# Kernel optimization log

Measured on AMD Instinct MI355X. Metric: run time of the kernel, lower is better.

Reference implementation:

```python
import jax, jax.numpy as jnp
import numpy as np

V = 25  # joints

def _normalize_adjacency_chain(adjacency: np.ndarray) -> np.ndarray:
    A = adjacency.astype(np.float32).copy()
    A += np.eye(A.shape[0], dtype=np.float32)
    row_sum = A.sum(axis=1, keepdims=True)
    row_sum[row_sum == 0.0] = 1.0
    return A / row_sum


def setup_inputs() -> dict:
    key = jax.random.key(0)
    k_x, k_w, k_b = jax.random.split(key, 3)
    N, C_in, C_out, T = 32, 256, 256, 300
    x = jax.random.normal(k_x, (N, C_in, V, T), dtype=jnp.float32)
    # chain adjacency over V joints, normalized with self-loops (module buffer)
    adj = np.zeros((V, V), dtype=np.float32)
    for i in range(V - 1):
        adj[i, i + 1] = 1.0
        adj[i + 1, i] = 1.0
    A = jnp.asarray(_normalize_adjacency_chain(adj))
    # 1x1 Conv2d params: weight (C_out, C_in), bias (C_out,)
    fan_in = C_in  # kernel 1x1
    bound = 1.0 / np.sqrt(fan_in)
    W = jax.random.uniform(k_w, (C_out, C_in), minval=-bound, maxval=bound, dtype=jnp.float32)
    b = jax.random.uniform(k_b, (C_out,), minval=-bound, maxval=bound, dtype=jnp.float32)
    return {"x": x, "A": A, "W": W, "b": b}


def reference(x, A, W, b):
    # x: (N, C, V, T); A: (V, V) row-normalized adjacency with self-loops
    agg = jnp.einsum('ncvt,vw->ncwt', x, A)          # graph aggregation
    out = jnp.einsum('ncvt,oc->novt', agg, W)        # 1x1 conv = channel GEMM
    return out + b[None, :, None, None]
```

## Files before the change

kernel.cpp:

```cpp
#include <hip/hip_runtime.h>

typedef unsigned short u16;
typedef unsigned int u32;
typedef __attribute__((ext_vector_type(8))) short short8;
typedef __attribute__((ext_vector_type(4))) float f32x4;
typedef __attribute__((ext_vector_type(2))) unsigned int u32x2;
typedef __attribute__((ext_vector_type(4))) unsigned int u32x4;

#define C_IN 256
#define C_OUT 256
#define VJ 25
#define TT 300
#define VT 7500
#define ROWBLKS 59
#define PERN_ELEMS (ROWBLKS * 4 * 128 * 64)
#define WB_ELEMS (256 * 256)

__device__ __forceinline__ u16 f2bf(float f) {
  u32 u = __float_as_uint(f);
  u32 r = (u + 0x7fffu + ((u >> 16) & 1u)) >> 16;
  return (u16)r;
}

__global__ void k0_wcast(const float* __restrict__ W, u16* __restrict__ Wb) {
  int i = (blockIdx.x * 256 + threadIdx.x) * 4;
  f32x4 w = *(const f32x4*)(W + i);
  u32x2 pk;
  pk[0] = (u32)f2bf(w[0]) | ((u32)f2bf(w[1]) << 16);
  pk[1] = (u32)f2bf(w[2]) | ((u32)f2bf(w[3]) << 16);
  *(u32x2*)(Wb + i) = pk;
}

__global__ __launch_bounds__(256) void k1_stencil(
    const float* __restrict__ x, const float* __restrict__ A,
    u16* __restrict__ aggT, int n0) {
  __shared__ float cw[25][4];
  __shared__ u16 agg_s[25 * 16 * 72];
  const int tid = threadIdx.x;
  const int tblk = blockIdx.x;
  const int cblk = blockIdx.y;
  const int nn = blockIdx.z;
  const int n = n0 + nn;

  if (tid < 25) {
    int w = tid;
    cw[w][0] = (w > 0) ? A[(w - 1) * 25 + w] : 0.0f;
    cw[w][1] = A[w * 25 + w];
    cw[w][2] = (w < 24) ? A[(w + 1) * 25 + w] : 0.0f;
  }
  __syncthreads();

  const int t_i = tid & 15;
  const int c_i = tid >> 4;
  const int t0 = tblk * 16 + t_i;
  const int tc = (t0 < TT) ? t0 : (TT - 1);

#pragma unroll
  for (int jp = 0; jp < 4; jp += 2) {
    const int cl = c_i * 4 + jp;
    const int c = cblk * 64 + cl;
    const float* xp0 = x + ((size_t)n * C_IN + c) * VT + tc;
    const float* xp1 = xp0 + VT;
    float xv0[25], xv1[25];
#pragma unroll
    for (int v = 0; v < 25; ++v) { xv0[v] = xp0[v * TT]; xv1[v] = xp1[v * TT]; }
#pragma unroll
    for (int w = 0; w < 25; ++w) {
      const int wm = (w > 0) ? w - 1 : 0;
      const int wp = (w < 24) ? w + 1 : 24;
      float a0 = cw[w][0], a1 = cw[w][1], a2 = cw[w][2];
      float r0 = xv0[wm] * a0 + xv0[w] * a1 + xv0[wp] * a2;
      float r1 = xv1[wm] * a0 + xv1[w] * a1 + xv1[wp] * a2;
      u32 pk = (u32)f2bf(r0) | ((u32)f2bf(r1) << 16);
      *(u32*)&agg_s[(w * 16 + t_i) * 72 + cl] = pk;
    }
  }
  __syncthreads();

  const int c8 = tid & 7;
  const int rb = tid >> 3;
  u16* dstn = aggT + (size_t)nn * PERN_ELEMS;
#pragma unroll
  for (int it = 0; it < 13; ++it) {
    int rr = it * 32 + rb;
    if (rr < 400) {
      int w = rr >> 4, ti = rr & 15;
      int t = tblk * 16 + ti;
      if (t < TT) {
        int g = w * TT + t;
        int rowblk = g >> 7, row_in = g & 127;
        u32x4 v = *(const u32x4*)&agg_s[(w * 16 + ti) * 72 + c8 * 8];
        *(u32x4*)(dstn + ((size_t)(rowblk * 4 + cblk) * 128 + row_in) * 64 + c8 * 8) = v;
      }
    }
  }
}

__global__ __launch_bounds__(256, 2) void k2_gemm(
    const u16* __restrict__ aggT, const u16* __restrict__ Wb,
    const float* __restrict__ bias, float* __restrict__ out, int n0) {
  __shared__ u16 As[128 * 64];
  __shared__ u16 Bs[128 * 64];
  const int tid = threadIdx.x;
  const int cb = blockIdx.x;
  const int ob = blockIdx.y;
  const int nn = blockIdx.z;
  const int n = n0 + nn;
  const int l = tid & 63;
  const int wv = tid >> 6;
  const int wm = wv & 1, wn = wv >> 1;
  const int m = l & 15, quad = l >> 4;
  f32x4 acc[4][4] = {};

  const u16* aggn = aggT + (size_t)nn * PERN_ELEMS + (size_t)cb * 4 * 8192;
  const u16* wbase = Wb + ob * 128 * 256;

  for (int kb = 0; kb < 4; ++kb) {
#pragma unroll
    for (int i = 0; i < 4; ++i) {
      int ch = i * 256 + tid;
      int row = ch >> 3, jp = ch & 7;
      int jd = jp ^ (row & 7);
      const u16* ga = wbase + row * 256 + kb * 64 + jd * 8;
      __builtin_amdgcn_global_load_lds((const __attribute__((address_space(1))) void*)ga,
                                       (__attribute__((address_space(3))) void*)&As[ch * 8],
                                       16, 0, 0);
      const u16* gb = aggn + kb * 8192 + row * 64 + jd * 8;
      __builtin_amdgcn_global_load_lds((const __attribute__((address_space(1))) void*)gb,
                                       (__attribute__((address_space(3))) void*)&Bs[ch * 8],
                                       16, 0, 0);
    }
    __syncthreads();
#pragma unroll
    for (int ks = 0; ks < 2; ++ks) {
      short8 af[4], bfr[4];
      int jj = ks * 4 + quad;
#pragma unroll
      for (int mi = 0; mi < 4; ++mi) {
        int row = wm * 64 + mi * 16 + m;
        af[mi] = *(const short8*)&As[row * 64 + ((jj ^ (row & 7)) * 8)];
      }
#pragma unroll
      for (int ni = 0; ni < 4; ++ni) {
        int row = wn * 64 + ni * 16 + m;
        bfr[ni] = *(const short8*)&Bs[row * 64 + ((jj ^ (row & 7)) * 8)];
      }
#pragma unroll
      for (int mi = 0; mi < 4; ++mi)
#pragma unroll
        for (int ni = 0; ni < 4; ++ni)
          acc[mi][ni] = __builtin_amdgcn_mfma_f32_16x16x32_bf16(af[mi], bfr[ni], acc[mi][ni], 0, 0, 0);
    }
    __syncthreads();
  }

  float* outn = out + (size_t)n * C_OUT * VT;
  const int colbase = cb * 128 + wn * 64 + m;
#pragma unroll
  for (int mi = 0; mi < 4; ++mi) {
    const int o0 = ob * 128 + wm * 64 + mi * 16 + quad * 4;
    float b0 = bias[o0], b1 = bias[o0 + 1], b2 = bias[o0 + 2], b3 = bias[o0 + 3];
#pragma unroll
    for (int ni = 0; ni < 4; ++ni) {
      int col = colbase + ni * 16;
      if (col < VT) {
        float* p = outn + (size_t)o0 * VT + col;
        p[0]          = acc[mi][ni][0] + b0;
        p[VT]         = acc[mi][ni][1] + b1;
        p[2 * VT]     = acc[mi][ni][2] + b2;
        p[3 * VT]     = acc[mi][ni][3] + b3;
      }
    }
  }
}

extern "C" void kernel_launch(void* const* d_in, const int* in_sizes, int n_in,
                              void* d_out, int out_size, void* d_ws, size_t ws_size,
                              hipStream_t stream) {
  (void)in_sizes; (void)n_in; (void)out_size;
  const float* x = (const float*)d_in[0];
  const float* A = (const float*)d_in[1];
  const float* W = (const float*)d_in[2];
  const float* b = (const float*)d_in[3];
  float* out = (float*)d_out;
  u16* wb = (u16*)d_ws;
  u16* aggT = wb + WB_ELEMS;

  const size_t pern_bytes = (size_t)PERN_ELEMS * 2;
  const size_t base_bytes = (size_t)WB_ELEMS * 2;
  int nchunk = 1;
  if (ws_size > base_bytes + pern_bytes) {
    size_t a = (ws_size - base_bytes) / pern_bytes;
    nchunk = (a >= 32) ? 32 : (int)a;
  }

  k0_wcast<<<64, 256, 0, stream>>>(W, wb);
  for (int n0 = 0; n0 < 32; n0 += nchunk) {
    int nc = 32 - n0; if (nc > nchunk) nc = nchunk;
    k1_stencil<<<dim3(19, 4, nc), 256, 0, stream>>>(x, A, aggT, n0);
    k2_gemm<<<dim3(59, 2, nc), 256, 0, stream>>>(aggT, wb, b, out, n0);
  }
}
```

Baseline: 514.5 us.

## Fuse graph stencil into GEMM, computing bf16 operands in registers

Replaces the separate stencil and GEMM kernels with one kernel where each lane computes the 3-tap graph aggregation directly from x and packs it into MFMA B fragments, while W fragments are loaded directly from global memory. This removes the workspace round trip of the bf16 intermediate and the per-chunk launches. It trades that for redundant neighbor loads of x, narrower x access segments, and no LDS staging of W, and it adds nontemporal output stores.

```diff
diff --git a/kernel.cpp b/kernel.cpp
--- a/kernel.cpp
+++ b/kernel.cpp
@@ -5,21 +5,15 @@
 typedef __attribute__((ext_vector_type(8))) short short8;
 typedef __attribute__((ext_vector_type(4))) float f32x4;
 typedef __attribute__((ext_vector_type(2))) unsigned int u32x2;
-typedef __attribute__((ext_vector_type(4))) unsigned int u32x4;
 
+#define TT 300
+#define VT 7500
 #define C_IN 256
 #define C_OUT 256
-#define VJ 25
-#define TT 300
-#define VT 7500
-#define ROWBLKS 59
-#define PERN_ELEMS (ROWBLKS * 4 * 128 * 64)
-#define WB_ELEMS (256 * 256)
 
 __device__ __forceinline__ u16 f2bf(float f) {
   u32 u = __float_as_uint(f);
-  u32 r = (u + 0x7fffu + ((u >> 16) & 1u)) >> 16;
-  return (u16)r;
+  return (u16)((u + 0x7fffu + ((u >> 16) & 1u)) >> 16);
 }
 
 __global__ void k0_wcast(const float* __restrict__ W, u16* __restrict__ Wb) {
@@ -31,144 +25,79 @@
   *(u32x2*)(Wb + i) = pk;
 }
 
-__global__ __launch_bounds__(256) void k1_stencil(
+__global__ __launch_bounds__(512) void k_fused(
     const float* __restrict__ x, const float* __restrict__ A,
-    u16* __restrict__ aggT, int n0) {
-  __shared__ float cw[25][4];
-  __shared__ u16 agg_s[25 * 16 * 72];
+    const u16* __restrict__ Wb, const float* __restrict__ bias,
+    float* __restrict__ out) {
   const int tid = threadIdx.x;
-  const int tblk = blockIdx.x;
-  const int cblk = blockIdx.y;
-  const int nn = blockIdx.z;
-  const int n = n0 + nn;
+  const int l = tid & 63, wv = tid >> 6;
+  const int gw = wv & 3, ow = wv >> 2;
+  const int quad = l >> 4, m16 = l & 15;
+  const int cb = blockIdx.x, n = blockIdx.y;
 
-  if (tid < 25) {
-    int w = tid;
-    cw[w][0] = (w > 0) ? A[(w - 1) * 25 + w] : 0.0f;
-    cw[w][1] = A[w * 25 + w];
-    cw[w][2] = (w < 24) ? A[(w + 1) * 25 + w] : 0.0f;
+  const float* xn = x + (size_t)n * C_IN * VT;
+
+  int gcol[2];
+  float ac[2][3];
+  const float* xb[2][3];
+#pragma unroll
+  for (int gt = 0; gt < 2; ++gt) {
+    int g = cb * 128 + gw * 32 + gt * 16 + m16;
+    gcol[gt] = g;
+    int gc = (g < VT) ? g : (VT - 1);
+    int w = gc / TT, t = gc - w * TT;
+    ac[gt][0] = (w > 0) ? A[(w - 1) * 25 + w] : 0.0f;
+    ac[gt][1] = A[w * 25 + w];
+    ac[gt][2] = (w < 24) ? A[(w + 1) * 25 + w] : 0.0f;
+    int wm = (w > 0) ? w - 1 : 0, wp = (w < 24) ? w + 1 : 24;
+    const float* base = xn + (size_t)(quad * 8) * VT + t;
+    xb[gt][0] = base + wm * TT;
+    xb[gt][1] = base + w * TT;
+    xb[gt][2] = base + wp * TT;
   }
-  __syncthreads();
 
-  const int t_i = tid & 15;
-  const int c_i = tid >> 4;
-  const int t0 = tblk * 16 + t_i;
-  const int tc = (t0 < TT) ? t0 : (TT - 1);
+  const u16* wrow = Wb + (size_t)(ow * 128 + m16) * C_IN + quad * 8;
 
+  f32x4 acc[8][2] = {};
+  for (int ks = 0; ks < 8; ++ks) {
+    short8 bf[2];
 #pragma unroll
-  for (int jp = 0; jp < 4; jp += 2) {
-    const int cl = c_i * 4 + jp;
-    const int c = cblk * 64 + cl;
-    const float* xp0 = x + ((size_t)n * C_IN + c) * VT + tc;
-    const float* xp1 = xp0 + VT;
-    float xv0[25], xv1[25];
+    for (int gt = 0; gt < 2; ++gt) {
 #pragma unroll
-    for (int v = 0; v < 25; ++v) { xv0[v] = xp0[v * TT]; xv1[v] = xp1[v * TT]; }
-#pragma unroll
-    for (int w = 0; w < 25; ++w) {
-      const int wm = (w > 0) ? w - 1 : 0;
-      const int wp = (w < 24) ? w + 1 : 24;
-      float a0 = cw[w][0], a1 = cw[w][1], a2 = cw[w][2];
-      float r0 = xv0[wm] * a0 + xv0[w] * a1 + xv0[wp] * a2;
-      float r1 = xv1[wm] * a0 + xv1[w] * a1 + xv1[wp] * a2;
-      u32 pk = (u32)f2bf(r0) | ((u32)f2bf(r1) << 16);
-      *(u32*)&agg_s[(w * 16 + t_i) * 72 + cl] = pk;
-    }
-  }
-  __syncthreads();
-
-  const int c8 = tid & 7;
-  const int rb = tid >> 3;
-  u16* dstn = aggT + (size_t)nn * PERN_ELEMS;
-#pragma unroll
-  for (int it = 0; it < 13; ++it) {
-    int rr = it * 32 + rb;
-    if (rr < 400) {
-      int w = rr >> 4, ti = rr & 15;
-      int t = tblk * 16 + ti;
-      if (t < TT) {
-        int g = w * TT + t;
-        int rowblk = g >> 7, row_in = g & 127;
-        u32x4 v = *(const u32x4*)&agg_s[(w * 16 + ti) * 72 + c8 * 8];
-        *(u32x4*)(dstn + ((size_t)(rowblk * 4 + cblk) * 128 + row_in) * 64 + c8 * 8) = v;
+      for (int j = 0; j < 8; ++j) {
+        size_t off = (size_t)(ks * 32 + j) * VT;
+        float xm = xb[gt][0][off];
+        float x0 = xb[gt][1][off];
+        float xp = xb[gt][2][off];
+        float r = ac[gt][0] * xm + ac[gt][1] * x0 + ac[gt][2] * xp;
+        bf[gt][j] = (short)f2bf(r);
       }
     }
-  }
-}
-
-__global__ __launch_bounds__(256, 2) void k2_gemm(
-    const u16* __restrict__ aggT, const u16* __restrict__ Wb,
-    const float* __restrict__ bias, float* __restrict__ out, int n0) {
-  __shared__ u16 As[128 * 64];
-  __shared__ u16 Bs[128 * 64];
-  const int tid = threadIdx.x;
-  const int cb = blockIdx.x;
-  const int ob = blockIdx.y;
-  const int nn = blockIdx.z;
-  const int n = n0 + nn;
-  const int l = tid & 63;
-  const int wv = tid >> 6;
-  const int wm = wv & 1, wn = wv >> 1;
-  const int m = l & 15, quad = l >> 4;
-  f32x4 acc[4][4] = {};
-
-  const u16* aggn = aggT + (size_t)nn * PERN_ELEMS + (size_t)cb * 4 * 8192;
-  const u16* wbase = Wb + ob * 128 * 256;
-
-  for (int kb = 0; kb < 4; ++kb) {
+    short8 af[8];
 #pragma unroll
-    for (int i = 0; i < 4; ++i) {
-      int ch = i * 256 + tid;
-      int row = ch >> 3, jp = ch & 7;
-      int jd = jp ^ (row & 7);
-      const u16* ga = wbase + row * 256 + kb * 64 + jd * 8;
-      __builtin_amdgcn_global_load_lds((const __attribute__((address_space(1))) void*)ga,
-                                       (__attribute__((address_space(3))) void*)&As[ch * 8],
-                                       16, 0, 0);
-      const u16* gb = aggn + kb * 8192 + row * 64 + jd * 8;
-      __builtin_amdgcn_global_load_lds((const __attribute__((address_space(1))) void*)gb,
-                                       (__attribute__((address_space(3))) void*)&Bs[ch * 8],
-                                       16, 0, 0);
-    }
-    __syncthreads();
+    for (int ot = 0; ot < 8; ++ot)
+      af[ot] = *(const short8*)(wrow + (size_t)(ot * 16) * C_IN + ks * 32);
 #pragma unroll
-    for (int ks = 0; ks < 2; ++ks) {
-      short8 af[4], bfr[4];
-      int jj = ks * 4 + quad;
+    for (int ot = 0; ot < 8; ++ot)
 #pragma unroll
-      for (int mi = 0; mi < 4; ++mi) {
-        int row = wm * 64 + mi * 16 + m;
-        af[mi] = *(const short8*)&As[row * 64 + ((jj ^ (row & 7)) * 8)];
-      }
-#pragma unroll
-      for (int ni = 0; ni < 4; ++ni) {
-        int row = wn * 64 + ni * 16 + m;
-        bfr[ni] = *(const short8*)&Bs[row * 64 + ((jj ^ (row & 7)) * 8)];
-      }
-#pragma unroll
-      for (int mi = 0; mi < 4; ++mi)
-#pragma unroll
-        for (int ni = 0; ni < 4; ++ni)
-          acc[mi][ni] = __builtin_amdgcn_mfma_f32_16x16x32_bf16(af[mi], bfr[ni], acc[mi][ni], 0, 0, 0);
-    }
-    __syncthreads();
+      for (int gt = 0; gt < 2; ++gt)
+        acc[ot][gt] = __builtin_amdgcn_mfma_f32_16x16x32_bf16(af[ot], bf[gt], acc[ot][gt], 0, 0, 0);
   }
 
   float* outn = out + (size_t)n * C_OUT * VT;
-  const int colbase = cb * 128 + wn * 64 + m;
 #pragma unroll
-  for (int mi = 0; mi < 4; ++mi) {
-    const int o0 = ob * 128 + wm * 64 + mi * 16 + quad * 4;
-    float b0 = bias[o0], b1 = bias[o0 + 1], b2 = bias[o0 + 2], b3 = bias[o0 + 3];
+  for (int ot = 0; ot < 8; ++ot) {
+    int o0 = ow * 128 + ot * 16 + quad * 4;
+    f32x4 bv = *(const f32x4*)(bias + o0);
 #pragma unroll
-    for (int ni = 0; ni < 4; ++ni) {
-      int col = colbase + ni * 16;
+    for (int gt = 0; gt < 2; ++gt) {
+      int col = gcol[gt];
       if (col < VT) {
         float* p = outn + (size_t)o0 * VT + col;
-        p[0]          = acc[mi][ni][0] + b0;
-        p[VT]         = acc[mi][ni][1] + b1;
-        p[2 * VT]     = acc[mi][ni][2] + b2;
-        p[3 * VT]     = acc[mi][ni][3] + b3;
+        __builtin_nontemporal_store(acc[ot][gt][0] + bv[0], p);
+        __builtin_nontemporal_store(acc[ot][gt][1] + bv[1], p + VT);
+        __builtin_nontemporal_store(acc[ot][gt][2] + bv[2], p + 2 * VT);
+        __builtin_nontemporal_store(acc[ot][gt][3] + bv[3], p + 3 * VT);
       }
     }
   }
@@ -177,27 +106,14 @@
 extern "C" void kernel_launch(void* const* d_in, const int* in_sizes, int n_in,
                               void* d_out, int out_size, void* d_ws, size_t ws_size,
                               hipStream_t stream) {
-  (void)in_sizes; (void)n_in; (void)out_size;
+  (void)in_sizes; (void)n_in; (void)out_size; (void)ws_size;
   const float* x = (const float*)d_in[0];
   const float* A = (const float*)d_in[1];
   const float* W = (const float*)d_in[2];
   const float* b = (const float*)d_in[3];
   float* out = (float*)d_out;
   u16* wb = (u16*)d_ws;
-  u16* aggT = wb + WB_ELEMS;
-
-  const size_t pern_bytes = (size_t)PERN_ELEMS * 2;
-  const size_t base_bytes = (size_t)WB_ELEMS * 2;
-  int nchunk = 1;
-  if (ws_size > base_bytes + pern_bytes) {
-    size_t a = (ws_size - base_bytes) / pern_bytes;
-    nchunk = (a >= 32) ? 32 : (int)a;
-  }
 
   k0_wcast<<<64, 256, 0, stream>>>(W, wb);
-  for (int n0 = 0; n0 < 32; n0 += nchunk) {
-    int nc = 32 - n0; if (nc > nchunk) nc = nchunk;
-    k1_stencil<<<dim3(19, 4, nc), 256, 0, stream>>>(x, A, aggT, n0);
-    k2_gemm<<<dim3(59, 2, nc), 256, 0, stream>>>(aggT, wb, b, out, n0);
-  }
+  k_fused<<<dim3(59, 32), 512, 0, stream>>>(x, A, wb, b, out);
 }
```

Result: slower. 779.7 us (+51.6%).
